# Kernel tuning notes

Hardware: AMD Instinct MI355X
Metric: run time of the kernel (lower is better)

Reference implementation:

```python
import jax, jax.numpy as jnp
import numpy as np

B, L, D = 4, 1024, 768
HH = 12            # BERT attention heads
E, M = 30, 60      # entities / mentions per sample
P = E * (E - 1)    # 870 head-tail entity pairs
R = 97             # relation classes
BLK = 64           # block_size
NH = D // BLK      # 12 EGAT heads / bilinear groups
MIN = 1e-10


def setup_inputs():
    key = jax.random.key(0)
    ks = jax.random.split(key, 16)
    context = jax.random.normal(ks[0], (B, L, D), jnp.float32) * 0.1
    attention = jax.random.uniform(ks[1], (B, HH, L, L), jnp.float32)
    attention = attention / attention.sum(-1, keepdims=True)  # row-stochastic like softmax attn
    pos = jax.random.randint(ks[2], (B, M), 0, L)
    mention_map = (jnp.arange(L)[None, None, :] == pos[..., None]).astype(jnp.float32)  # [B,M,L] one-hot
    entity_map = (jnp.arange(M)[None, :] // 2 == jnp.arange(E)[:, None]).astype(jnp.float32)
    entity_map = jnp.broadcast_to(entity_map[None], (B, E, M))  # entity e owns mentions 2e,2e+1
    pairs = np.array([(i, j) for i in range(E) for j in range(E) if i != j], np.int64)
    hts = jnp.broadcast_to(jnp.asarray(pairs)[None], (B, P, 2))
    w = lambda k, s: jax.random.normal(k, s, jnp.float32) * 0.02
    return dict(
        context=context, attention=attention, mention_map=mention_map,
        entity_map=entity_map, hts=hts,
        W_h=w(ks[3], (2 * D, D)), b_h=jnp.zeros((D,), jnp.float32),
        W_t=w(ks[4], (2 * D, D)), b_t=jnp.zeros((D,), jnp.float32),
        W_node=w(ks[5], (D, NH * BLK)),
        W_ni=w(ks[6], (D, NH * BLK)), W_nj=w(ks[7], (D, NH * BLK)),
        W_fij=w(ks[8], (D, NH * BLK)), egat_bias=jnp.zeros((NH * BLK,), jnp.float32),
        attn_vec=w(ks[9], (NH, BLK)),
        W_rel=w(ks[10], (D * BLK, R)), b_rel=jnp.zeros((R,), jnp.float32),
    )


def reference(context, attention, mention_map, entity_map, hts,
              W_h, b_h, W_t, b_t, W_node, W_ni, W_nj, W_fij,
              egat_bias, attn_vec, W_rel, b_rel):
    bidx = jnp.arange(B)[:, None]
    ht_mask = (hts.sum(-1) != 0)[..., None].astype(context.dtype)  # [B,P,1]

    # ---- log-sum-exp entity pooling over mentions (get_ht) ----
    mention = jnp.exp(jnp.einsum('bml,bld->bmd', mention_map, context))  # [B,M,D]
    ent = jnp.einsum('bem,bmd->bed', entity_map, mention)                # [B,E,D]
    empty = entity_map.sum(-1, keepdims=True) == 0
    entity = jnp.log(jnp.where(empty, 1.0, ent))                          # [B,E,D]

    # ---- attention-weighted context pooling ----
    em = jnp.einsum('bem,bml->bel', entity_map, mention_map)             # entity -> token map
    em = em / (em.sum(-1, keepdims=True) + MIN)
    ea = jnp.einsum('bel,bhlm->behm', em, attention)                     # [B,E,HH,L]
    ah = ea[bidx, hts[..., 0]]                                            # [B,P,HH,L]
    at = ea[bidx, hts[..., 1]]
    ca = (ah * at).sum(2)                                                 # [B,P,L]
    ca = ca / (ca.sum(-1, keepdims=True) + MIN)
    context_info = jnp.einsum('bpl,bld->bpd', ca, context) * ht_mask      # [B,P,D]

    # ---- batched graph: all hts pairs are edges, plus self loops ----
    N = B * E
    off = (jnp.arange(B) * E)[:, None]
    src = jnp.concatenate([(hts[..., 0] + off).reshape(-1), jnp.arange(N)])
    dst = jnp.concatenate([(hts[..., 1] + off).reshape(-1), jnp.arange(N)])
    x = entity.reshape(N, D)
    efeat = jnp.concatenate([context_info.reshape(B * P, D), x], axis=0)  # pair edges then self loops

    # ---- EGATConv ----
    f_ni = (x @ W_ni).reshape(N, NH, BLK)
    f_nj = (x @ W_nj).reshape(N, NH, BLK)
    f_fij = (efeat @ W_fij).reshape(-1, NH, BLK)
    f_out = f_ni[src] + f_nj[dst] + f_fij + egat_bias.reshape(NH, BLK)    # [Etot,NH,BLK]
    e = jax.nn.leaky_relu(f_out, 0.2)
    scores = (e * attn_vec[None]).sum(-1)                                  # [Etot,NH]
    smax = jax.ops.segment_max(scores, dst, num_segments=N)
    ex = jnp.exp(scores - smax[dst])
    ssum = jax.ops.segment_sum(ex, dst, num_segments=N)
    alpha = ex / ssum[dst]                                                 # edge softmax over in-edges
    msg = (x @ W_node).reshape(N, NH, BLK)[src] * alpha[..., None]
    nodes = jax.ops.segment_sum(msg, dst, num_segments=N)                  # [N,NH,BLK]

    edge_ctx = f_out[:B * P].reshape(B, P, D)                              # get_res (all edges kept, order preserved)
    node_feat = nodes.reshape(B, E, D)

    # ---- get_new_ht + dense + tanh ----
    new_h = jnp.tanh(jnp.concatenate([node_feat[bidx, hts[..., 0]], edge_ctx], -1) @ W_h + b_h)
    new_t = jnp.tanh(jnp.concatenate([node_feat[bidx, hts[..., 1]], edge_ctx], -1) @ W_t + b_t)

    # ---- group biLinear relation classifier ----
    a = new_h.reshape(B, P, NH, BLK)
    b = new_t.reshape(B, P, NH, BLK)
    bl = jnp.einsum('bpkx,bpky->bpkxy', a, b).reshape(B, P, NH * BLK * BLK)
    return bl @ W_rel + b_rel                                              # [B,P,R]
```

## Files before the change

### kernel.cpp

```cpp
#include <hip/hip_runtime.h>
#include <math.h>

#define BB 4
#define LLL 1024
#define DDD 768
#define HHH 12
#define EEE 30
#define MMM 60
#define PPP 870
#define RRR 97
#define NNODE 120
#define NPAIR 3480
#define NEDGE 3600
#define FMIN 1e-10f

typedef __attribute__((ext_vector_type(8))) __bf16 bf16x8;
typedef __attribute__((ext_vector_type(8))) short short8;
typedef __attribute__((ext_vector_type(8))) _Float16 f16x8;
typedef __attribute__((ext_vector_type(4))) float f32x4;
typedef __attribute__((ext_vector_type(4))) unsigned short u16x4;

static __device__ __forceinline__ unsigned short f2bf(float v) {
  return __builtin_bit_cast(unsigned short, (__bf16)v);
}
static __device__ __forceinline__ unsigned short f2h(float v) {
  return __builtin_bit_cast(unsigned short, (_Float16)v);
}
static __device__ __forceinline__ float bf2f(unsigned short u) {
  unsigned int x = ((unsigned int)u) << 16;
  return __builtin_bit_cast(float, x);
}

struct PrepArgs {
  const float *Wrel, *context, *mmap, *emap;
  const float *wsrc[6];
  unsigned short *tW, *ctxT, *xb;
  unsigned short *wdst[6];
  int *nzl, *nzc;
  float *nzw;
};

#define NB_WPREP 768
#define NB_CTX   (24 * 32 * BB)
#define NB_WT    (24 * 48 * 6)
#define NB_ENT   NNODE
#define NB_EM    NNODE

static __device__ void body_wprep(int c, const float* __restrict__ Wrel,
                                  unsigned short* __restrict__ tW) {
  __shared__ float w_s[64][98];
  int tid = threadIdx.x;
  for (int idx = tid; idx < 64 * 97; idx += 256) {
    int y = idx / 97, r = idx - y * 97;
    w_s[y][r] = Wrel[(size_t)(c * 64 + y) * RRR + r];
  }
  __syncthreads();
  for (int odx = tid; odx < 8192; odx += 256) {
    int nt = odx >> 10, h = (odx >> 9) & 1, lane = (odx >> 3) & 63, i = odx & 7;
    int y = 32 * h + 8 * (lane >> 4) + i;
    int r = nt * 16 + (lane & 15);
    float v = (r < RRR) ? w_s[y][r] : 0.f;
    tW[(size_t)c * 8192 + odx] = f2h(v);
  }
}

static __device__ void body_transpose(int bx, int by, const float* __restrict__ s,
                                      unsigned short* __restrict__ d, int R, int C) {
  __shared__ float t_s[32][33];
  int c0 = bx * 32, r0 = by * 32;
  int tx = threadIdx.x & 31, ty = threadIdx.x >> 5;
  #pragma unroll
  for (int i = 0; i < 4; i++)
    t_s[ty + i * 8][tx] = s[(size_t)(r0 + ty + i * 8) * C + c0 + tx];
  __syncthreads();
  #pragma unroll
  for (int i = 0; i < 4; i++)
    d[(size_t)(c0 + ty + i * 8) * R + r0 + tx] = f2bf(t_s[tx][ty + i * 8]);
}

static __device__ void body_entity(int be, const float* __restrict__ ctx,
                                   const float* __restrict__ mmap,
                                   const float* __restrict__ emap,
                                   unsigned short* __restrict__ xb) {
  __shared__ int s_cnt;
  __shared__ int s_l[16];
  __shared__ float s_w[16];
  int b = be / EEE;
  int tid = threadIdx.x;
  float acc[3] = {0.f, 0.f, 0.f};
  float csum = 0.f;
  for (int m = 0; m < MMM; m++) {
    float wm = emap[(size_t)be * MMM + m];
    csum += wm;
    if (wm == 0.f) continue;
    if (tid == 0) s_cnt = 0;
    __syncthreads();
    const float* mrow = mmap + ((size_t)b * MMM + m) * LLL;
    #pragma unroll
    for (int q = 0; q < 4; q++) {
      int l = tid + 256 * q;
      float w = mrow[l];
      if (w != 0.f) {
        int i = atomicAdd(&s_cnt, 1);
        if (i < 16) { s_l[i] = l; s_w[i] = w; }
      }
    }
    __syncthreads();
    int c = min(s_cnt, 16);
    float dot[3] = {0.f, 0.f, 0.f};
    for (int i = 0; i < c; i++) {
      const float* cr = ctx + ((size_t)b * LLL + s_l[i]) * DDD;
      float w = s_w[i];
      #pragma unroll
      for (int q = 0; q < 3; q++) dot[q] += w * cr[tid + 256 * q];
    }
    #pragma unroll
    for (int q = 0; q < 3; q++) acc[q] += wm * expf(dot[q]);
  }
  bool empty = (csum == 0.f);
  #pragma unroll
  for (int q = 0; q < 3; q++)
    xb[(size_t)be * DDD + tid + 256 * q] = f2bf(empty ? 0.f : logf(acc[q]));
}

static __device__ void body_em(int be, const float* __restrict__ emap,
                               const float* __restrict__ mmap,
                               int* __restrict__ nzl, float* __restrict__ nzw,
                               int* __restrict__ nzc) {
  __shared__ float em_s[1024];
  __shared__ float red[256];
  int b = be / EEE;
  int tid = threadIdx.x;
  float acc[4] = {0.f, 0.f, 0.f, 0.f};
  for (int m = 0; m < MMM; m++) {
    float w = emap[(size_t)be * MMM + m];
    if (w != 0.f) {
      const float* mr = mmap + ((size_t)b * MMM + m) * LLL;
      #pragma unroll
      for (int q = 0; q < 4; q++) acc[q] += w * mr[tid + 256 * q];
    }
  }
  red[tid] = acc[0] + acc[1] + acc[2] + acc[3];
  __syncthreads();
  for (int st = 128; st > 0; st >>= 1) {
    if (tid < st) red[tid] += red[tid + st];
    __syncthreads();
  }
  float inv = 1.f / (red[0] + FMIN);
  #pragma unroll
  for (int q = 0; q < 4; q++) em_s[tid + 256 * q] = acc[q] * inv;
  __syncthreads();
  if (tid < 64) {
    int base = 0;
    for (int l0 = 0; l0 < LLL; l0 += 64) {
      float w = em_s[l0 + tid];
      unsigned long long mb = __ballot(w != 0.f);
      int pre = __popcll(mb & ((1ull << tid) - 1ull));
      if (w != 0.f) {
        nzl[be * LLL + base + pre] = l0 + tid;
        nzw[be * LLL + base + pre] = w;
      }
      base += __popcll(mb);
    }
    if (tid == 0) nzc[be] = base;
  }
}

__global__ __launch_bounds__(256) void k_prep(PrepArgs a) {
  int bid = blockIdx.x;
  if (bid < NB_WPREP) {
    body_wprep(bid, a.Wrel, a.tW);
    return;
  }
  bid -= NB_WPREP;
  if (bid < NB_CTX) {
    int bx = bid % 24, by = (bid / 24) % 32, bz = bid / (24 * 32);
    body_transpose(bx, by, a.context + (size_t)bz * LLL * DDD,
                   a.ctxT + (size_t)bz * DDD * LLL, LLL, DDD);
    return;
  }
  bid -= NB_CTX;
  if (bid < NB_WT) {
    int bx = bid % 24, by = (bid / 24) % 48, bz = bid / (24 * 48);
    int R = (bz < 4) ? DDD : 2 * DDD;
    if (by * 32 < R) body_transpose(bx, by, a.wsrc[bz], a.wdst[bz], R, DDD);
    return;
  }
  bid -= NB_WT;
  if (bid < NB_ENT) {
    body_entity(bid, a.context, a.mmap, a.emap, a.xb);
    return;
  }
  bid -= NB_ENT;
  body_em(bid, a.emap, a.mmap, a.nzl, a.nzw, a.nzc);
}

__global__ __launch_bounds__(256) void k_ea(const float* __restrict__ attn,
                                            const int* __restrict__ nzl,
                                            const float* __restrict__ nzw,
                                            const int* __restrict__ nzc,
                                            unsigned short* __restrict__ ea) {
  int e = blockIdx.x, h = blockIdx.y, b = blockIdx.z;
  int be = b * EEE + e;
  int cnt = nzc[be];
  float acc[4] = {0.f, 0.f, 0.f, 0.f};
  for (int i = 0; i < cnt; i++) {
    int l = nzl[be * LLL + i];
    float w = nzw[be * LLL + i];
    const float* ar = attn + (((size_t)b * HHH + h) * LLL + l) * LLL;
    #pragma unroll
    for (int q = 0; q < 4; q++) acc[q] += w * ar[threadIdx.x + 256 * q];
  }
  unsigned short* er = ea + ((size_t)be * HHH + h) * LLL;
  #pragma unroll
  for (int q = 0; q < 4; q++) er[threadIdx.x + 256 * q] = f2bf(acc[q]);
}

__global__ __launch_bounds__(256) void k_ca(const unsigned short* __restrict__ ea,
                                            const int* __restrict__ hts,
                                            unsigned short* __restrict__ cab,
                                            const float* __restrict__ brel,
                                            float* __restrict__ out) {
  int bp = blockIdx.x;
  int b = bp / PPP;
  int hs = hts[bp * 2 + 0], ts = hts[bp * 2 + 1];
  int tid = threadIdx.x;
  if (tid < RRR) out[(size_t)bp * RRR + tid] = brel[tid];
  const unsigned short* eh = ea + (size_t)(b * EEE + hs) * HHH * LLL;
  const unsigned short* et = ea + (size_t)(b * EEE + ts) * HHH * LLL;
  float v[4] = {0.f, 0.f, 0.f, 0.f};
  #pragma unroll
  for (int h = 0; h < HHH; h++) {
    u16x4 hv = *(const u16x4*)&eh[h * LLL + tid * 4];
    u16x4 tv = *(const u16x4*)&et[h * LLL + tid * 4];
    #pragma unroll
    for (int q = 0; q < 4; q++) v[q] += bf2f(hv[q]) * bf2f(tv[q]);
  }
  __shared__ float red[256];
  red[tid] = v[0] + v[1] + v[2] + v[3];
  __syncthreads();
  for (int st = 128; st > 0; st >>= 1) {
    if (tid < st) red[tid] += red[tid + st];
    __syncthreads();
  }
  float inv = 1.f / (red[0] + FMIN);
  u16x4 o;
  #pragma unroll
  for (int q = 0; q < 4; q++) o[q] = f2bf(v[q] * inv);
  *(u16x4*)&cab[(size_t)bp * LLL + tid * 4] = o;
}

struct MGArgs {
  const unsigned short *A, *A2, *BT0, *BT1, *BT2, *nodes;
  float *C0, *C1, *C2;
  unsigned short *Cb;
  unsigned short *Ch, *Ct;
  const float *bias0, *bias1;
  const float *fni, *fnj, *ebias, *avec;
  float *scores;
  const int *hts;
  int M, K;
};

template <int MODE>
__global__ __launch_bounds__(256) void k_mgemm(MGArgs g) {
  __shared__ unsigned short As[3][64 * 64];
  __shared__ unsigned short Bs[3][64 * 64];
  int tid = threadIdx.x;
  int lane = tid & 63;
  int wv = tid >> 6;
  int l15 = lane & 15, l4 = lane >> 4;
  int wr = wv >> 1, wc = wv & 1;
  int row0 = blockIdx.x * 64, col0 = blockIdx.y * 64;
  int bz = blockIdx.z;
  int K = g.K;

  const unsigned short* BTp;
  if (MODE == 0) BTp = g.BT0 + (size_t)bz * DDD * LLL;
  else if (MODE == 1) BTp = bz == 0 ? g.BT0 : (bz == 1 ? g.BT1 : g.BT2);
  else if (MODE == 2) BTp = g.BT0;
  else BTp = bz ? g.BT1 : g.BT0;

  int sgg = (lane & 7) ^ ((lane >> 3) & 7);
  int srsub = lane >> 3;

  const unsigned short* gaA[2];
  const unsigned short* gaA2[2];
  const unsigned short* gaB[2];
  #pragma unroll
  for (int jj = 0; jj < 2; jj++) {
    int j = wv * 2 + jj;
    int row = j * 8 + srsub;
    int grow = row0 + row; if (grow >= g.M) grow = g.M - 1;
    if (MODE == 0) {
      gaA[jj] = g.A + ((size_t)(bz * PPP) + grow) * LLL + sgg * 8;
    } else if (MODE == 1) {
      gaA[jj] = g.A + (size_t)grow * DDD + sgg * 8;
    } else if (MODE == 2) {
      gaA[jj] = (grow < NPAIR) ? g.A + (size_t)grow * DDD + sgg * 8
                               : g.A2 + (size_t)(grow - NPAIR) * DDD + sgg * 8;
    } else {
      int b = grow / PPP;
      int node = b * EEE + g.hts[grow * 2 + bz];
      gaA[jj] = g.nodes + (size_t)node * DDD + sgg * 8;
      gaA2[jj] = g.A2 + (size_t)grow * DDD + sgg * 8;
    }
    gaB[jj] = BTp + (size_t)(col0 + row) * K + sgg * 8;
  }

  auto stage = [&](int buf, int t) {
    int k = t * 64;
    #pragma unroll
    for (int jj = 0; jj < 2; jj++) {
      int j = wv * 2 + jj;
      const unsigned short* ga;
      if (MODE == 3) ga = (k < DDD) ? gaA[jj] + k : gaA2[jj] + (k - DDD);
      else ga = gaA[jj] + k;
      const unsigned short* gb = gaB[jj] + k;
      __builtin_amdgcn_global_load_lds(
          (const __attribute__((address_space(1))) unsigned int*)ga,
          (__attribute__((address_space(3))) unsigned int*)&As[buf][j * 512],
          16, 0, 0);
      __builtin_amdgcn_global_load_lds(
          (const __attribute__((address_space(1))) unsigned int*)gb,
          (__attribute__((address_space(3))) unsigned int*)&Bs[buf][j * 512],
          16, 0, 0);
    }
  };

  f32x4 zero = {0.f, 0.f, 0.f, 0.f};
  f32x4 acc[2][2];
  #pragma unroll
  for (int m = 0; m < 2; m++)
    #pragma unroll
    for (int n = 0; n < 2; n++) acc[m][n] = zero;

  int nt = K / 64;
  stage(0, 0);
  stage(1, 1);
  asm volatile("s_waitcnt vmcnt(4)" ::: "memory");
  __builtin_amdgcn_s_barrier();

  int cur = 0;
  for (int t = 0; t < nt; t++) {
    if (t + 2 < nt) {
      int nxt2 = cur - 1; if (nxt2 < 0) nxt2 = 2;
      stage(nxt2, t + 2);
    }
    short8 af[2][2], bfr[2][2];
    #pragma unroll
    for (int ks = 0; ks < 2; ks++) {
      #pragma unroll
      for (int m = 0; m < 2; m++) {
        int row = wr * 32 + m * 16 + l15;
        int phys = (ks * 4 + l4) ^ (row & 7);
        af[ks][m] = *(const short8*)&As[cur][row * 64 + phys * 8];
      }
      #pragma unroll
      for (int n = 0; n < 2; n++) {
        int row = wc * 32 + n * 16 + l15;
        int phys = (ks * 4 + l4) ^ (row & 7);
        bfr[ks][n] = *(const short8*)&Bs[cur][row * 64 + phys * 8];
      }
    }
    #pragma unroll
    for (int ks = 0; ks < 2; ks++)
      #pragma unroll
      for (int m = 0; m < 2; m++)
        #pragma unroll
        for (int n = 0; n < 2; n++)
          acc[m][n] = __builtin_amdgcn_mfma_f32_16x16x32_bf16(af[ks][m], bfr[ks][n], acc[m][n], 0, 0, 0);
    if (t + 1 < nt) {
      if (t + 2 < nt) asm volatile("s_waitcnt vmcnt(4)" ::: "memory");
      else            asm volatile("s_waitcnt vmcnt(0)" ::: "memory");
      __builtin_amdgcn_s_barrier();
    }
    cur += 1; if (cur == 3) cur = 0;
  }

  float* score_s = (float*)&As[0][0];
  if (MODE == 2) {
    if (tid < 64) score_s[tid] = 0.f;
    __syncthreads();
  }

  #pragma unroll
  for (int m = 0; m < 2; m++) {
    int rbase = row0 + wr * 32 + m * 16 + l4 * 4;
    #pragma unroll
    for (int n = 0; n < 2; n++) {
      int col = col0 + wc * 32 + n * 16 + l15;
      #pragma unroll
      for (int q = 0; q < 4; q++) {
        int r = rbase + q;
        if (r >= g.M) continue;
        float v = acc[m][n][q];
        if (MODE == 0) {
          size_t grow = (size_t)bz * PPP + r;
          int h0 = g.hts[grow * 2 + 0], h1 = g.hts[grow * 2 + 1];
          float mk = (h0 + h1 != 0) ? 1.f : 0.f;
          g.Cb[grow * DDD + col] = f2bf(v * mk);
        } else if (MODE == 1) {
          float* C = bz == 0 ? g.C0 : (bz == 1 ? g.C1 : g.C2);
          C[(size_t)r * DDD + col] = v;
        } else if (MODE == 2) {
          int srcn, dstn;
          if (r < NPAIR) {
            int bb = r / PPP;
            srcn = bb * EEE + g.hts[r * 2 + 0];
            dstn = bb * EEE + g.hts[r * 2 + 1];
          } else {
            srcn = dstn = r - NPAIR;
          }
          float vv = v + g.fni[(size_t)srcn * DDD + col] +
                     g.fnj[(size_t)dstn * DDD + col] + g.ebias[col];
          g.Cb[(size_t)r * DDD + col] = f2bf(vv);
          float lrv = vv > 0.f ? vv : 0.2f * vv;
          atomicAdd(&score_s[r - row0], lrv * g.avec[col]);
        } else {
          unsigned short* C = bz ? g.Ct : g.Ch;
          const float* bias = bz ? g.bias1 : g.bias0;
          C[(size_t)r * DDD + col] = f2h(tanhf(v + bias[col]));
        }
      }
    }
  }

  if (MODE == 2) {
    __syncthreads();
    if (tid < 64) {
      int r = row0 + tid;
      if (r < g.M) g.scores[r * HHH + blockIdx.y] = score_s[tid];
    }
  }
}

#define ECAP 256
__global__ __launch_bounds__(256) void k_agg(const float* __restrict__ scores,
                                             const float* __restrict__ fnode,
                                             const int* __restrict__ hts,
                                             unsigned short* __restrict__ nodesb) {
  __shared__ int cnt;
  __shared__ int elist[ECAP], slist[ECAP];
  __shared__ float smax[HHH], ssum[HHH];
  __shared__ float alpha[ECAP * HHH];
  int n = blockIdx.x, tid = threadIdx.x;
  if (tid == 0) cnt = 0;
  __syncthreads();
  for (int e = tid; e < NEDGE; e += 256) {
    int srcn, dstn;
    if (e < NPAIR) {
      int b = e / PPP;
      srcn = b * EEE + hts[e * 2 + 0];
      dstn = b * EEE + hts[e * 2 + 1];
    } else {
      srcn = dstn = e - NPAIR;
    }
    if (dstn == n) {
      int i = atomicAdd(&cnt, 1);
      if (i < ECAP) { elist[i] = e; slist[i] = srcn; }
    }
  }
  __syncthreads();
  int c = min(cnt, ECAP);
  if (tid < HHH) {
    float m = -1e30f;
    for (int i = 0; i < c; i++) m = fmaxf(m, scores[elist[i] * HHH + tid]);
    smax[tid] = m;
    float s = 0.f;
    for (int i = 0; i < c; i++) s += expf(scores[elist[i] * HHH + tid] - m);
    ssum[tid] = s;
  }
  __syncthreads();
  for (int t = tid; t < c * HHH; t += 256) {
    int i = t / HHH, h = t - i * HHH;
    alpha[t] = expf(scores[elist[i] * HHH + h] - smax[h]) / ssum[h];
  }
  __syncthreads();
  for (int j = tid; j < DDD; j += 256) {
    int h = j >> 6;
    float acc = 0.f;
    for (int i = 0; i < c; i++)
      acc += alpha[i * HHH + h] * fnode[(size_t)slist[i] * DDD + j];
    nodesb[(size_t)n * DDD + j] = f2bf(acc);
  }
}

__global__ __launch_bounds__(256) void k_bilinear_mfma(
    const unsigned short* __restrict__ newh, const unsigned short* __restrict__ newt,
    const unsigned short* __restrict__ tW, float* __restrict__ out) {
  __shared__ unsigned short a_s[64][64];
  int tid = threadIdx.x;
  int lane = tid & 63;
  int wv = tid >> 6;
  int l15 = lane & 15, l4 = lane >> 4;
  int bid = blockIdx.x;
  int kg = bid / 55, pt = bid - kg * 55;
  bool use1 = ((wv + 4) * 16) < RRR;

  {
    int pl = tid >> 2, xq = (tid & 3) * 16;
    int prow = pt * 64 + pl; if (prow >= NPAIR) prow = NPAIR - 1;
    const unsigned short* src = newh + (size_t)prow * DDD + kg * 64 + xq;
    #pragma unroll
    for (int half16 = 0; half16 < 2; half16++) {
      u16x4 v0 = *(const u16x4*)(src + half16 * 8);
      u16x4 v1 = *(const u16x4*)(src + half16 * 8 + 4);
      #pragma unroll
      for (int i = 0; i < 4; i++) {
        a_s[xq + half16 * 8 + i][pl] = v0[i];
        a_s[xq + half16 * 8 + 4 + i][pl] = v1[i];
      }
    }
  }

  f16x8 bfrag[4][2];
  #pragma unroll
  for (int t = 0; t < 4; t++) {
    int prow = pt * 64 + t * 16 + l15; if (prow >= NPAIR) prow = NPAIR - 1;
    const unsigned short* src = newt + (size_t)prow * DDD + kg * 64 + 8 * l4;
    #pragma unroll
    for (int h = 0; h < 2; h++)
      bfrag[t][h] = __builtin_bit_cast(f16x8, *(const uint4*)(src + h * 32));
  }
  __syncthreads();

  f32x4 zero = {0.f, 0.f, 0.f, 0.f};
  f32x4 acc[4][2];
  #pragma unroll
  for (int t = 0; t < 4; t++) { acc[t][0] = zero; acc[t][1] = zero; }

  const unsigned short* wp = tW + (size_t)(kg * 64) * 8192 + lane * 8;
  int o00 = (wv * 2 + 0) << 9;
  int o01 = (wv * 2 + 1) << 9;
  int o10 = ((wv + 4) * 2 + 0) << 9;
  int o11 = ((wv + 4) * 2 + 1) << 9;

  auto loadw = [&](uint4* wf, int x) {
    const unsigned short* p = wp + (size_t)x * 8192;
    wf[0] = *(const uint4*)(p + o00);
    wf[1] = *(const uint4*)(p + o01);
    if (use1) {
      wf[2] = *(const uint4*)(p + o10);
      wf[3] = *(const uint4*)(p + o11);
    }
  };
  auto step = [&](const uint4* wf, int x) {
    f16x8 a8[4];
    #pragma unroll
    for (int t = 0; t < 4; t++) {
      unsigned int av = a_s[x][t * 16 + l15];
      unsigned int aw = (av << 16) | av;
      uint4 ab = {aw, aw, aw, aw};
      a8[t] = __builtin_bit_cast(f16x8, ab);
    }
    #pragma unroll
    for (int h = 0; h < 2; h++) {
      f16x8 w0 = __builtin_bit_cast(f16x8, wf[h]);
      f16x8 w1 = __builtin_bit_cast(f16x8, wf[2 + h]);
      #pragma unroll
      for (int t = 0; t < 4; t++) {
        f16x8 gv = a8[t] * bfrag[t][h];
        acc[t][0] = __builtin_amdgcn_mfma_f32_16x16x32_f16(gv, w0, acc[t][0], 0, 0, 0);
        if (use1)
          acc[t][1] = __builtin_amdgcn_mfma_f32_16x16x32_f16(gv, w1, acc[t][1], 0, 0, 0);
      }
    }
  };

  uint4 wa[4], wb[4];
  loadw(wa, 0);
  for (int xx = 0; xx < 64; xx += 2) {
    loadw(wb, xx + 1);
    step(wa, xx);
    if (xx + 2 < 64) loadw(wa, xx + 2);
    step(wb, xx + 1);
  }

  #pragma unroll
  for (int n = 0; n < 2; n++) {
    int r = (wv + 4 * n) * 16 + l15;
    if (r >= RRR) continue;
    #pragma unroll
    for (int t = 0; t < 4; t++) {
      int pbase = pt * 64 + t * 16 + l4 * 4;
      #pragma unroll
      for (int q = 0; q < 4; q++) {
        int p = pbase + q;
        if (p < NPAIR) atomicAdd(&out[(size_t)p * RRR + r], acc[t][n][q]);
      }
    }
  }
}

extern "C" void kernel_launch(void* const* d_in, const int* in_sizes, int n_in,
                              void* d_out, int out_size, void* d_ws, size_t ws_size,
                              hipStream_t stream) {
  const float* context   = (const float*)d_in[0];
  const float* attention = (const float*)d_in[1];
  const float* mmap      = (const float*)d_in[2];
  const float* emap      = (const float*)d_in[3];
  const int*   hts       = (const int*)d_in[4];
  const float* W_h       = (const float*)d_in[5];
  const float* b_h       = (const float*)d_in[6];
  const float* W_t       = (const float*)d_in[7];
  const float* b_t       = (const float*)d_in[8];
  const float* W_node    = (const float*)d_in[9];
  const float* W_ni      = (const float*)d_in[10];
  const float* W_nj      = (const float*)d_in[11];
  const float* W_fij     = (const float*)d_in[12];
  const float* egat_bias = (const float*)d_in[13];
  const float* attn_vec  = (const float*)d_in[14];
  const float* W_rel     = (const float*)d_in[15];
  const float* b_rel     = (const float*)d_in[16];
  float* out = (float*)d_out;

  float* ws = (float*)d_ws;
  size_t o = 0;
  auto alloc = [&](size_t n) { size_t r = o; o += (n + 63) & ~(size_t)63; return r; };
  auto halloc = [&](size_t nshorts) { return alloc((nshorts + 1) / 2); };
  size_t o_xb      = halloc((size_t)NNODE * DDD);
  size_t o_ea      = halloc((size_t)BB * EEE * HHH * LLL);
  size_t o_cab     = halloc((size_t)NPAIR * LLL);
  size_t o_ctxT    = halloc((size_t)BB * DDD * LLL);
  size_t o_wtni    = halloc((size_t)DDD * DDD);
  size_t o_wtnj    = halloc((size_t)DDD * DDD);
  size_t o_wtnode  = halloc((size_t)DDD * DDD);
  size_t o_wtfij   = halloc((size_t)DDD * DDD);
  size_t o_wth     = halloc((size_t)DDD * 2 * DDD);
  size_t o_wtt     = halloc((size_t)DDD * 2 * DDD);
  size_t o_cinfob  = halloc((size_t)NPAIR * DDD);
  size_t o_fni     = alloc((size_t)NNODE * DDD);
  size_t o_fnj     = alloc((size_t)NNODE * DDD);
  size_t o_fnode   = alloc((size_t)NNODE * DDD);
  size_t o_foutb   = halloc((size_t)NEDGE * DDD);
  size_t o_scores  = alloc((size_t)NEDGE * HHH);
  size_t o_nodesb  = halloc((size_t)NNODE * DDD);
  size_t o_newh    = halloc((size_t)NPAIR * DDD);
  size_t o_newt    = halloc((size_t)NPAIR * DDD);
  size_t o_nzl     = alloc((size_t)BB * EEE * LLL);
  size_t o_nzw     = alloc((size_t)BB * EEE * LLL);
  size_t o_nzc     = alloc(128);
  size_t o_tw      = halloc((size_t)768 * 8192);
  (void)ws_size;

  unsigned short* xb     = (unsigned short*)(ws + o_xb);
  unsigned short* ea     = (unsigned short*)(ws + o_ea);
  unsigned short* cab    = (unsigned short*)(ws + o_cab);
  unsigned short* ctxT   = (unsigned short*)(ws + o_ctxT);
  unsigned short* wtni   = (unsigned short*)(ws + o_wtni);
  unsigned short* wtnj   = (unsigned short*)(ws + o_wtnj);
  unsigned short* wtnode = (unsigned short*)(ws + o_wtnode);
  unsigned short* wtfij  = (unsigned short*)(ws + o_wtfij);
  unsigned short* wth    = (unsigned short*)(ws + o_wth);
  unsigned short* wtt    = (unsigned short*)(ws + o_wtt);
  unsigned short* cinfob = (unsigned short*)(ws + o_cinfob);
  float* fni     = ws + o_fni;
  float* fnj     = ws + o_fnj;
  float* fnode   = ws + o_fnode;
  unsigned short* foutb  = (unsigned short*)(ws + o_foutb);
  float* scores  = ws + o_scores;
  unsigned short* nodesb = (unsigned short*)(ws + o_nodesb);
  unsigned short* newh   = (unsigned short*)(ws + o_newh);
  unsigned short* newt   = (unsigned short*)(ws + o_newt);
  int*   nzl     = (int*)(ws + o_nzl);
  float* nzw     = ws + o_nzw;
  int*   nzc     = (int*)(ws + o_nzc);
  unsigned short* tW = (unsigned short*)(ws + o_tw);

  PrepArgs pa;
  pa.Wrel = W_rel; pa.context = context; pa.mmap = mmap; pa.emap = emap;
  pa.wsrc[0] = W_ni;  pa.wdst[0] = wtni;
  pa.wsrc[1] = W_nj;  pa.wdst[1] = wtnj;
  pa.wsrc[2] = W_node; pa.wdst[2] = wtnode;
  pa.wsrc[3] = W_fij; pa.wdst[3] = wtfij;
  pa.wsrc[4] = W_h;   pa.wdst[4] = wth;
  pa.wsrc[5] = W_t;   pa.wdst[5] = wtt;
  pa.tW = tW; pa.ctxT = ctxT; pa.xb = xb;
  pa.nzl = nzl; pa.nzw = nzw; pa.nzc = nzc;
  k_prep<<<NB_WPREP + NB_CTX + NB_WT + NB_ENT + NB_EM, 256, 0, stream>>>(pa);

  k_ea<<<dim3(EEE, HHH, BB), 256, 0, stream>>>(attention, nzl, nzw, nzc, ea);
  k_ca<<<BB * PPP, 256, 0, stream>>>(ea, hts, cab, b_rel, out);

  MGArgs gc = {};
  gc.A = cab; gc.BT0 = ctxT; gc.Cb = cinfob; gc.hts = hts; gc.M = PPP; gc.K = LLL;
  k_mgemm<0><<<dim3(14, 12, BB), 256, 0, stream>>>(gc);

  MGArgs gf = {};
  gf.A = xb; gf.BT0 = wtni; gf.BT1 = wtnj; gf.BT2 = wtnode;
  gf.C0 = fni; gf.C1 = fnj; gf.C2 = fnode; gf.M = NNODE; gf.K = DDD;
  k_mgemm<1><<<dim3(2, 12, 3), 256, 0, stream>>>(gf);

  MGArgs gj = {};
  gj.A = cinfob; gj.A2 = xb; gj.BT0 = wtfij; gj.Cb = foutb;
  gj.fni = fni; gj.fnj = fnj; gj.ebias = egat_bias; gj.avec = attn_vec;
  gj.scores = scores; gj.hts = hts; gj.M = NEDGE; gj.K = DDD;
  k_mgemm<2><<<dim3(57, 12, 1), 256, 0, stream>>>(gj);

  k_agg<<<NNODE, 256, 0, stream>>>(scores, fnode, hts, nodesb);

  MGArgs gn = {};
  gn.A2 = foutb; gn.nodes = nodesb; gn.BT0 = wth; gn.BT1 = wtt;
  gn.bias0 = b_h; gn.bias1 = b_t; gn.Ch = newh; gn.Ct = newt;
  gn.hts = hts; gn.M = NPAIR; gn.K = 2 * DDD;
  k_mgemm<3><<<dim3(55, 12, 2), 256, 0, stream>>>(gn);

  k_bilinear_mfma<<<55 * 12, 256, 0, stream>>>(newh, newt, tW, out);
}
```

Before: 227.1 us.

## Factor node projection out of new_h/new_t GEMM and merge independent GEMM launches

The head/tail dense layer is split algebraically. The node-feature half is computed once per node (120 rows) in a small GEMM and then gathered and added in the epilogue of the pair GEMM, which now runs with K=768 instead of 1536. The context-attention GEMM and the three node projection GEMMs are merged into one launch (MODE 5) through the z-dimension. The EGAT score reduction now uses wave shuffles before one shared-memory atomic per row, instead of an atomic per element. This adds an extra launch and fp32 nodeW traffic, and the MODE 5 grid wastes early-exit blocks.

```diff
diff --git a/kernel.cpp b/kernel.cpp
--- a/kernel.cpp
+++ b/kernel.cpp
@@ -251,15 +251,16 @@
 }
 
 struct MGArgs {
-  const unsigned short *A, *A2, *BT0, *BT1, *BT2, *nodes;
+  const unsigned short *A, *A2, *BT0, *BT1, *BT2, *BT3;
   float *C0, *C1, *C2;
-  unsigned short *Cb;
-  unsigned short *Ch, *Ct;
+  const float *nodeW;
+  float *nodeWout;
+  unsigned short *Cb, *Ch, *Ct;
   const float *bias0, *bias1;
   const float *fni, *fnj, *ebias, *avec;
   float *scores;
   const int *hts;
-  int M, K;
+  int M, K, ldb, koffB;
 };
 
 template <int MODE>
@@ -271,13 +272,20 @@
   int wv = tid >> 6;
   int l15 = lane & 15, l4 = lane >> 4;
   int wr = wv >> 1, wc = wv & 1;
+  int bz = blockIdx.z;
+
+  bool isC = true; int zz = 0;
+  if (MODE == 5) {
+    isC = bz < 4; zz = bz - 4;
+    if (!isC && blockIdx.x >= 2) return;
+  }
+  int K = g.K, M = g.M, ldb = g.ldb, koffB = g.koffB;
+  if (MODE == 5) { K = isC ? LLL : DDD; M = isC ? PPP : NNODE; ldb = K; koffB = 0; }
   int row0 = blockIdx.x * 64, col0 = blockIdx.y * 64;
-  int bz = blockIdx.z;
-  int K = g.K;
 
   const unsigned short* BTp;
-  if (MODE == 0) BTp = g.BT0 + (size_t)bz * DDD * LLL;
-  else if (MODE == 1) BTp = bz == 0 ? g.BT0 : (bz == 1 ? g.BT1 : g.BT2);
+  if (MODE == 5) BTp = isC ? g.BT0 + (size_t)bz * DDD * LLL
+                           : (zz == 0 ? g.BT1 : (zz == 1 ? g.BT2 : g.BT3));
   else if (MODE == 2) BTp = g.BT0;
   else BTp = bz ? g.BT1 : g.BT0;
 
@@ -285,27 +293,22 @@
   int srsub = lane >> 3;
 
   const unsigned short* gaA[2];
-  const unsigned short* gaA2[2];
   const unsigned short* gaB[2];
   #pragma unroll
   for (int jj = 0; jj < 2; jj++) {
     int j = wv * 2 + jj;
     int row = j * 8 + srsub;
-    int grow = row0 + row; if (grow >= g.M) grow = g.M - 1;
-    if (MODE == 0) {
-      gaA[jj] = g.A + ((size_t)(bz * PPP) + grow) * LLL + sgg * 8;
-    } else if (MODE == 1) {
-      gaA[jj] = g.A + (size_t)grow * DDD + sgg * 8;
+    int grow = row0 + row; if (grow >= M) grow = M - 1;
+    if (MODE == 5) {
+      gaA[jj] = isC ? g.A + ((size_t)(bz * PPP) + grow) * LLL + sgg * 8
+                    : g.A2 + (size_t)grow * DDD + sgg * 8;
     } else if (MODE == 2) {
       gaA[jj] = (grow < NPAIR) ? g.A + (size_t)grow * DDD + sgg * 8
                                : g.A2 + (size_t)(grow - NPAIR) * DDD + sgg * 8;
     } else {
-      int b = grow / PPP;
-      int node = b * EEE + g.hts[grow * 2 + bz];
-      gaA[jj] = g.nodes + (size_t)node * DDD + sgg * 8;
-      gaA2[jj] = g.A2 + (size_t)grow * DDD + sgg * 8;
-    }
-    gaB[jj] = BTp + (size_t)(col0 + row) * K + sgg * 8;
+      gaA[jj] = g.A + (size_t)grow * DDD + sgg * 8;
+    }
+    gaB[jj] = BTp + (size_t)(col0 + row) * ldb + koffB + sgg * 8;
   }
 
   auto stage = [&](int buf, int t) {
@@ -313,16 +316,12 @@
     #pragma unroll
     for (int jj = 0; jj < 2; jj++) {
       int j = wv * 2 + jj;
-      const unsigned short* ga;
-      if (MODE == 3) ga = (k < DDD) ? gaA[jj] + k : gaA2[jj] + (k - DDD);
-      else ga = gaA[jj] + k;
-      const unsigned short* gb = gaB[jj] + k;
       __builtin_amdgcn_global_load_lds(
-          (const __attribute__((address_space(1))) unsigned int*)ga,
+          (const __attribute__((address_space(1))) unsigned int*)(gaA[jj] + k),
           (__attribute__((address_space(3))) unsigned int*)&As[buf][j * 512],
           16, 0, 0);
       __builtin_amdgcn_global_load_lds(
-          (const __attribute__((address_space(1))) unsigned int*)gb,
+          (const __attribute__((address_space(1))) unsigned int*)(gaB[jj] + k),
           (__attribute__((address_space(3))) unsigned int*)&Bs[buf][j * 512],
           16, 0, 0);
     }
@@ -384,6 +383,7 @@
     __syncthreads();
   }
 
+  float sp[2][4] = {};
   #pragma unroll
   for (int m = 0; m < 2; m++) {
     int rbase = row0 + wr * 32 + m * 16 + l4 * 4;
@@ -393,16 +393,18 @@
       #pragma unroll
       for (int q = 0; q < 4; q++) {
         int r = rbase + q;
-        if (r >= g.M) continue;
+        if (r >= M) continue;
         float v = acc[m][n][q];
-        if (MODE == 0) {
-          size_t grow = (size_t)bz * PPP + r;
-          int h0 = g.hts[grow * 2 + 0], h1 = g.hts[grow * 2 + 1];
-          float mk = (h0 + h1 != 0) ? 1.f : 0.f;
-          g.Cb[grow * DDD + col] = f2bf(v * mk);
-        } else if (MODE == 1) {
-          float* C = bz == 0 ? g.C0 : (bz == 1 ? g.C1 : g.C2);
-          C[(size_t)r * DDD + col] = v;
+        if (MODE == 5) {
+          if (isC) {
+            size_t grow = (size_t)bz * PPP + r;
+            int h0 = g.hts[grow * 2 + 0], h1 = g.hts[grow * 2 + 1];
+            float mk = (h0 + h1 != 0) ? 1.f : 0.f;
+            g.Cb[grow * DDD + col] = f2bf(v * mk);
+          } else {
+            float* C = zz == 0 ? g.C0 : (zz == 1 ? g.C1 : g.C2);
+            C[(size_t)r * DDD + col] = v;
+          }
         } else if (MODE == 2) {
           int srcn, dstn;
           if (r < NPAIR) {
@@ -416,21 +418,39 @@
                      g.fnj[(size_t)dstn * DDD + col] + g.ebias[col];
           g.Cb[(size_t)r * DDD + col] = f2bf(vv);
           float lrv = vv > 0.f ? vv : 0.2f * vv;
-          atomicAdd(&score_s[r - row0], lrv * g.avec[col]);
+          sp[m][q] += lrv * g.avec[col];
+        } else if (MODE == 4) {
+          g.nodeWout[((size_t)bz * NNODE + r) * DDD + col] = v;
         } else {
+          int bb = r / PPP;
+          int node = bb * EEE + g.hts[r * 2 + bz];
+          const float* bias = bz ? g.bias1 : g.bias0;
+          float v2 = v + g.nodeW[((size_t)bz * NNODE + node) * DDD + col] + bias[col];
           unsigned short* C = bz ? g.Ct : g.Ch;
-          const float* bias = bz ? g.bias1 : g.bias0;
-          C[(size_t)r * DDD + col] = f2h(tanhf(v + bias[col]));
+          C[(size_t)r * DDD + col] = f2h(tanhf(v2));
         }
       }
     }
   }
 
   if (MODE == 2) {
+    #pragma unroll
+    for (int m = 0; m < 2; m++) {
+      #pragma unroll
+      for (int q = 0; q < 4; q++) {
+        float s = sp[m][q];
+        s += __shfl_xor(s, 1);
+        s += __shfl_xor(s, 2);
+        s += __shfl_xor(s, 4);
+        s += __shfl_xor(s, 8);
+        int r = row0 + wr * 32 + m * 16 + l4 * 4 + q;
+        if (l15 == 0 && r < M) atomicAdd(&score_s[r - row0], s);
+      }
+    }
     __syncthreads();
     if (tid < 64) {
       int r = row0 + tid;
-      if (r < g.M) g.scores[r * HHH + blockIdx.y] = score_s[tid];
+      if (r < M) g.scores[r * HHH + blockIdx.y] = score_s[tid];
     }
   }
 }
@@ -636,6 +656,7 @@
   size_t o_foutb   = halloc((size_t)NEDGE * DDD);
   size_t o_scores  = alloc((size_t)NEDGE * HHH);
   size_t o_nodesb  = halloc((size_t)NNODE * DDD);
+  size_t o_nodew   = alloc((size_t)2 * NNODE * DDD);
   size_t o_newh    = halloc((size_t)NPAIR * DDD);
   size_t o_newt    = halloc((size_t)NPAIR * DDD);
   size_t o_nzl     = alloc((size_t)BB * EEE * LLL);
@@ -661,6 +682,7 @@
   unsigned short* foutb  = (unsigned short*)(ws + o_foutb);
   float* scores  = ws + o_scores;
   unsigned short* nodesb = (unsigned short*)(ws + o_nodesb);
+  float* nodeW   = ws + o_nodew;
   unsigned short* newh   = (unsigned short*)(ws + o_newh);
   unsigned short* newt   = (unsigned short*)(ws + o_newt);
   int*   nzl     = (int*)(ws + o_nzl);
@@ -683,28 +705,32 @@
   k_ea<<<dim3(EEE, HHH, BB), 256, 0, stream>>>(attention, nzl, nzw, nzc, ea);
   k_ca<<<BB * PPP, 256, 0, stream>>>(ea, hts, cab, b_rel, out);
 
-  MGArgs gc = {};
-  gc.A = cab; gc.BT0 = ctxT; gc.Cb = cinfob; gc.hts = hts; gc.M = PPP; gc.K = LLL;
-  k_mgemm<0><<<dim3(14, 12, BB), 256, 0, stream>>>(gc);
-
-  MGArgs gf = {};
-  gf.A = xb; gf.BT0 = wtni; gf.BT1 = wtnj; gf.BT2 = wtnode;
-  gf.C0 = fni; gf.C1 = fnj; gf.C2 = fnode; gf.M = NNODE; gf.K = DDD;
-  k_mgemm<1><<<dim3(2, 12, 3), 256, 0, stream>>>(gf);
-
-  MGArgs gj = {};
-  gj.A = cinfob; gj.A2 = xb; gj.BT0 = wtfij; gj.Cb = foutb;
-  gj.fni = fni; gj.fnj = fnj; gj.ebias = egat_bias; gj.avec = attn_vec;
-  gj.scores = scores; gj.hts = hts; gj.M = NEDGE; gj.K = DDD;
-  k_mgemm<2><<<dim3(57, 12, 1), 256, 0, stream>>>(gj);
+  MGArgs g5 = {};
+  g5.A = cab; g5.A2 = xb;
+  g5.BT0 = ctxT; g5.BT1 = wtni; g5.BT2 = wtnj; g5.BT3 = wtnode;
+  g5.Cb = cinfob; g5.C0 = fni; g5.C1 = fnj; g5.C2 = fnode;
+  g5.hts = hts;
+  k_mgemm<5><<<dim3(14, 12, 7), 256, 0, stream>>>(g5);
+
+  MGArgs g2 = {};
+  g2.A = cinfob; g2.A2 = xb; g2.BT0 = wtfij; g2.Cb = foutb;
+  g2.fni = fni; g2.fnj = fnj; g2.ebias = egat_bias; g2.avec = attn_vec;
+  g2.scores = scores; g2.hts = hts;
+  g2.M = NEDGE; g2.K = DDD; g2.ldb = DDD; g2.koffB = 0;
+  k_mgemm<2><<<dim3(57, 12, 1), 256, 0, stream>>>(g2);
 
   k_agg<<<NNODE, 256, 0, stream>>>(scores, fnode, hts, nodesb);
 
-  MGArgs gn = {};
-  gn.A2 = foutb; gn.nodes = nodesb; gn.BT0 = wth; gn.BT1 = wtt;
-  gn.bias0 = b_h; gn.bias1 = b_t; gn.Ch = newh; gn.Ct = newt;
-  gn.hts = hts; gn.M = NPAIR; gn.K = 2 * DDD;
-  k_mgemm<3><<<dim3(55, 12, 2), 256, 0, stream>>>(gn);
+  MGArgs g4 = {};
+  g4.A = nodesb; g4.BT0 = wth; g4.BT1 = wtt; g4.nodeWout = nodeW;
+  g4.M = NNODE; g4.K = DDD; g4.ldb = 2 * DDD; g4.koffB = 0;
+  k_mgemm<4><<<dim3(2, 12, 2), 256, 0, stream>>>(g4);
+
+  MGArgs g3 = {};
+  g3.A = foutb; g3.BT0 = wth; g3.BT1 = wtt; g3.nodeW = nodeW;
+  g3.bias0 = b_h; g3.bias1 = b_t; g3.Ch = newh; g3.Ct = newt; g3.hts = hts;
+  g3.M = NPAIR; g3.K = DDD; g3.ldb = 2 * DDD; g3.koffB = DDD;
+  k_mgemm<3><<<dim3(55, 12, 2), 256, 0, stream>>>(g3);
 
   k_bilinear_mfma<<<55 * 12, 256, 0, stream>>>(newh, newt, tW, out);
 }
```

Result: faster. 208.2 us (-8.4%).
